# Optimization experiments

Hardware: AMD Instinct MI355X
Metric: run time of the kernel (lower is better)

The kernel has to match this reference:

```python
import jax, jax.numpy as jnp
import numpy as np

WINDOW = 1024
UNITS = 128


def setup_inputs() -> dict:
    key = jax.random.key(0)
    k1, k2, k3 = jax.random.split(key, 3)
    input_tensor = jax.random.normal(k1, (1, UNITS), dtype=jnp.float32)
    state = jax.random.normal(k2, (UNITS, WINDOW), dtype=jnp.float32)
    w = jax.random.normal(k3, (2 * UNITS + 1, UNITS), dtype=jnp.float32) * 0.05
    b = jnp.zeros((UNITS,), dtype=jnp.float32)
    return {"input_tensor": input_tensor, "state": state, "w": w, "b": b}


def reference(input_tensor, state, w, b):
    U, W = state.shape
    # state @ state_shift (shift matrix with ones on subdiagonal) == drop first column
    shifted_state = state[:, 1:]                          # [U, W-1]
    new_state = jnp.concatenate([shifted_state, input_tensor.T], axis=-1)  # [U, W]
    fs = new_state.T                                      # flip_state: [W, U]

    # h_i[i,j,:] = fs[j];  h_j[i,j,:] = fs[i]
    # se_ij = concat([h_i, h_j, <h_i,h_j>], -1); sim = se_ij @ w + b
    # Split w so we never materialize the [W,W,2U+1] concat tensor:
    w_hi = w[:U]        # [U, U] multiplies h_i (fs[j])
    w_hj = w[U:2 * U]   # [U, U] multiplies h_j (fs[i])
    w_dot = w[2 * U]    # [U]    multiplies the pairwise dot product

    proj_hi = fs @ w_hi                                   # [W, U], indexed by j
    proj_hj = fs @ w_hj                                   # [W, U], indexed by i
    d = fs @ fs.T                                         # [W, W] pairwise dots

    # sim[i,j,u] = proj_hi[j,u] + proj_hj[i,u] + d[i,j]*w_dot[u] + b[u]
    sim = proj_hi[None, :, :] + proj_hj[:, None, :] + d[:, :, None] * w_dot + b  # [W,W,U]
    a = jax.nn.softmax(sim, axis=1)                       # softmax over j

    # c[i,u] = sum_j h_i[i,j,u] * a[i,j,u] = sum_j fs[j,u] * a[i,j,u]
    c = jnp.einsum('ju,iju->iu', fs, a)                   # [W, U]
    c_last = c[-1].reshape(1, U)                          # [1, U]
    return c_last
```

## Files before the change

### kernel.cpp

```cpp
#include <hip/hip_runtime.h>


constexpr int U = 128;
constexpr int W = 1024;

__global__ __launch_bounds__(256) void rsa_last_kernel(
    const float* __restrict__ input,
    const float* __restrict__ state,
    const float* __restrict__ w,
    float* __restrict__ out)
{
    const int u    = blockIdx.x;
    const int t    = threadIdx.x;
    const int lane = t & 63;
    const int wid  = t >> 6;

    __shared__ float v[U];
    __shared__ float spv[4];
    __shared__ float smax[4];
    __shared__ float ssum[4];
    __shared__ float snum[4];

    const float wdot_u = w[2 * U * U + u];

    float pv = 0.0f;
    if (t < U) {
        float inv = input[t];
        float vt  = fmaf(wdot_u, inv, w[t * U + u]);
        v[t] = vt;
        pv   = vt * inv;
    }
    #pragma unroll
    for (int o = 32; o > 0; o >>= 1) pv += __shfl_down(pv, o, 64);
    if (lane == 0) spv[wid] = pv;
    __syncthreads();

    float acc0 = 0.f, acc1 = 0.f, acc2 = 0.f, acc3 = 0.f;
    const float4* sp = (const float4*)(state) + t;
    #pragma unroll 8
    for (int k = 0; k < U; ++k) {
        const float  vk = v[k];
        const float4 f  = sp[k * (W / 4)];
        acc0 = fmaf(vk, f.x, acc0);
        acc1 = fmaf(vk, f.y, acc1);
        acc2 = fmaf(vk, f.z, acc2);
        acc3 = fmaf(vk, f.w, acc3);
    }
    if (t == 0) acc0 = spv[0] + spv[1];

    float lm = fmaxf(fmaxf(acc0, acc1), fmaxf(acc2, acc3));
    #pragma unroll
    for (int o = 32; o > 0; o >>= 1) lm = fmaxf(lm, __shfl_down(lm, o, 64));
    if (lane == 0) smax[wid] = lm;
    __syncthreads();
    const float m = fmaxf(fmaxf(smax[0], smax[1]), fmaxf(smax[2], smax[3]));

    float4 g = *((const float4*)(state + (size_t)u * W) + t);
    if (t == 0) g.x = input[u];

    const float e0 = __expf(acc0 - m);
    const float e1 = __expf(acc1 - m);
    const float e2 = __expf(acc2 - m);
    const float e3 = __expf(acc3 - m);
    float ls = e0 + e1 + e2 + e3;
    float ln = fmaf(g.x, e0, fmaf(g.y, e1, fmaf(g.z, e2, g.w * e3)));
    #pragma unroll
    for (int o = 32; o > 0; o >>= 1) {
        ls += __shfl_down(ls, o, 64);
        ln += __shfl_down(ln, o, 64);
    }
    if (lane == 0) { ssum[wid] = ls; snum[wid] = ln; }
    __syncthreads();

    if (t == 0) {
        const float denom = ssum[0] + ssum[1] + ssum[2] + ssum[3];
        const float numer = snum[0] + snum[1] + snum[2] + snum[3];
        out[u] = numer / denom;
    }
}

extern "C" void kernel_launch(void* const* d_in, const int* in_sizes, int n_in,
                              void* d_out, int out_size, void* d_ws, size_t ws_size,
                              hipStream_t stream) {
    const float* input = (const float*)d_in[0];
    const float* state = (const float*)d_in[1];
    const float* w     = (const float*)d_in[2];
    float* out = (float*)d_out;

    rsa_last_kernel<<<dim3(U), dim3(256), 0, stream>>>(input, state, w, out);
}
```

Measured before the change: 66.53 us.

## Use one thread per window column and drop softmax max pass

Each block now launches 1024 threads, one per window column, instead of 256 threads that each handle four columns through float4 loads. Column indexing is changed to follow the shifted state directly. The softmax max-reduction and its barrier are removed, so exponentials are taken of raw logits. This raises the number of waves available to hide memory latency, at the cost of narrower per-thread loads and a risk of overflow when logits are large.

```diff
diff --git a/kernel.cpp b/kernel.cpp
--- a/kernel.cpp
+++ b/kernel.cpp
@@ -4,7 +4,7 @@
 constexpr int U = 128;
 constexpr int W = 1024;
 
-__global__ __launch_bounds__(256) void rsa_last_kernel(
+__global__ __launch_bounds__(1024, 4) void rsa_last_kernel(
     const float* __restrict__ input,
     const float* __restrict__ state,
     const float* __restrict__ w,
@@ -13,69 +13,69 @@
     const int u    = blockIdx.x;
     const int t    = threadIdx.x;
     const int lane = t & 63;
-    const int wid  = t >> 6;
+    const int wv   = t >> 6;
 
-    __shared__ float v[U];
-    __shared__ float spv[4];
-    __shared__ float smax[4];
-    __shared__ float ssum[4];
-    __shared__ float snum[4];
+    __shared__ float4 v4[U / 4];
+    __shared__ float  pvred[2];
+    __shared__ float  red[16][2];
 
     const float wdot_u = w[2 * U * U + u];
 
-    float pv = 0.0f;
     if (t < U) {
-        float inv = input[t];
-        float vt  = fmaf(wdot_u, inv, w[t * U + u]);
-        v[t] = vt;
-        pv   = vt * inv;
+        const float ik = input[t];
+        const float vt = fmaf(wdot_u, ik, w[t * U + u]);
+        ((float*)v4)[t] = vt;
+        float pv = vt * ik;
+        #pragma unroll
+        for (int o = 32; o > 0; o >>= 1) pv += __shfl_down(pv, o, 64);
+        if (lane == 0) pvred[wv] = pv;
     }
-    #pragma unroll
-    for (int o = 32; o > 0; o >>= 1) pv += __shfl_down(pv, o, 64);
-    if (lane == 0) spv[wid] = pv;
     __syncthreads();
 
-    float acc0 = 0.f, acc1 = 0.f, acc2 = 0.f, acc3 = 0.f;
-    const float4* sp = (const float4*)(state) + t;
-    #pragma unroll 8
-    for (int k = 0; k < U; ++k) {
-        const float  vk = v[k];
-        const float4 f  = sp[k * (W / 4)];
-        acc0 = fmaf(vk, f.x, acc0);
-        acc1 = fmaf(vk, f.y, acc1);
-        acc2 = fmaf(vk, f.z, acc2);
-        acc3 = fmaf(vk, f.w, acc3);
+    const int   col = (t < W - 1) ? (t + 1) : 0;
+    const float* cp = state + col;
+    float acc = 0.0f;
+    #pragma unroll
+    for (int kc = 0; kc < U / 4; ++kc) {
+        const float4 vk = v4[kc];
+        const float f0 = cp[(4 * kc + 0) * W];
+        const float f1 = cp[(4 * kc + 1) * W];
+        const float f2 = cp[(4 * kc + 2) * W];
+        const float f3 = cp[(4 * kc + 3) * W];
+        acc = fmaf(vk.x, f0, acc);
+        acc = fmaf(vk.y, f1, acc);
+        acc = fmaf(vk.z, f2, acc);
+        acc = fmaf(vk.w, f3, acc);
     }
-    if (t == 0) acc0 = spv[0] + spv[1];
 
-    float lm = fmaxf(fmaxf(acc0, acc1), fmaxf(acc2, acc3));
-    #pragma unroll
-    for (int o = 32; o > 0; o >>= 1) lm = fmaxf(lm, __shfl_down(lm, o, 64));
-    if (lane == 0) smax[wid] = lm;
-    __syncthreads();
-    const float m = fmaxf(fmaxf(smax[0], smax[1]), fmaxf(smax[2], smax[3]));
+    float g;
+    if (t < W - 1) {
+        g = state[(size_t)u * W + col];
+    } else {
+        g   = input[u];
+        acc = pvred[0] + pvred[1];
+    }
 
-    float4 g = *((const float4*)(state + (size_t)u * W) + t);
-    if (t == 0) g.x = input[u];
-
-    const float e0 = __expf(acc0 - m);
-    const float e1 = __expf(acc1 - m);
-    const float e2 = __expf(acc2 - m);
-    const float e3 = __expf(acc3 - m);
-    float ls = e0 + e1 + e2 + e3;
-    float ln = fmaf(g.x, e0, fmaf(g.y, e1, fmaf(g.z, e2, g.w * e3)));
+    const float e = __expf(acc);
+    float den = e;
+    float num = g * e;
     #pragma unroll
     for (int o = 32; o > 0; o >>= 1) {
-        ls += __shfl_down(ls, o, 64);
-        ln += __shfl_down(ln, o, 64);
+        den += __shfl_down(den, o, 64);
+        num += __shfl_down(num, o, 64);
     }
-    if (lane == 0) { ssum[wid] = ls; snum[wid] = ln; }
+    if (lane == 0) { red[wv][0] = den; red[wv][1] = num; }
     __syncthreads();
 
-    if (t == 0) {
-        const float denom = ssum[0] + ssum[1] + ssum[2] + ssum[3];
-        const float numer = snum[0] + snum[1] + snum[2] + snum[3];
-        out[u] = numer / denom;
+    if (wv == 0) {
+        float d2 = (lane < 16) ? red[lane][0] : 0.0f;
+        float n2 = (lane < 16) ? red[lane][1] : 0.0f;
+        #pragma unroll
+        for (int o = 8; o > 0; o >>= 1) {
+            d2 += __shfl_down(d2, o, 64);
+            n2 += __shfl_down(n2, o, 64);
+        }
+        if (lane == 0) out[u] = n2 / d2;
     }
 }
 
@@ -87,5 +87,5 @@
     const float* w     = (const float*)d_in[2];
     float* out = (float*)d_out;
 
-    rsa_last_kernel<<<dim3(U), dim3(256), 0, stream>>>(input, state, w, out);
+    rsa_last_kernel<<<dim3(U), dim3(1024), 0, stream>>>(input, state, w, out);
 }
```

New measurement: 111.5 us. 67.6% more time.

## Compute four output units per block, reusing state loads; drop softmax max pass

Applied to the files above, without the earlier changes.

Each block now produces four output units. Every state float4 loaded in the 128-step dot-product loop feeds 16 FMAs across four accumulator vectors instead of 4. This cuts the number of times the shared 512KB state matrix is streamed from 128 passes to 32. The softmax max-reduction and its barrier are removed, so exponentials are taken on the raw logits. That is exact in value but can overflow for large logits. The grid shrinks to 32 blocks, which lowers parallelism on a many-CU device.

```diff
diff --git a/kernel.cpp b/kernel.cpp
--- a/kernel.cpp
+++ b/kernel.cpp
@@ -10,73 +10,109 @@
     const float* __restrict__ w,
     float* __restrict__ out)
 {
-    const int u    = blockIdx.x;
+    const int u0   = blockIdx.x * 4;
     const int t    = threadIdx.x;
     const int lane = t & 63;
-    const int wid  = t >> 6;
+    const int wv   = t >> 6;
 
-    __shared__ float v[U];
-    __shared__ float spv[4];
-    __shared__ float smax[4];
-    __shared__ float ssum[4];
-    __shared__ float snum[4];
+    __shared__ __align__(16) float4 v4[U];
+    __shared__ float  s1023r[2][4];
+    __shared__ float4 s1023;
+    __shared__ float  red[4][8];
+    __shared__ float  fin[8];
 
-    const float wdot_u = w[2 * U * U + u];
+    const float4 wd4 = *(const float4*)&w[2 * U * U + u0];
+    if (t < U) {
+        const float  ik = input[t];
+        const float4 wh = *(const float4*)&w[t * U + u0];
+        float4 vk;
+        vk.x = fmaf(wd4.x, ik, wh.x);
+        vk.y = fmaf(wd4.y, ik, wh.y);
+        vk.z = fmaf(wd4.z, ik, wh.z);
+        vk.w = fmaf(wd4.w, ik, wh.w);
+        v4[t] = vk;
+        float p0 = vk.x * ik, p1 = vk.y * ik, p2 = vk.z * ik, p3 = vk.w * ik;
+        #pragma unroll
+        for (int o = 32; o > 0; o >>= 1) {
+            p0 += __shfl_down(p0, o, 64);
+            p1 += __shfl_down(p1, o, 64);
+            p2 += __shfl_down(p2, o, 64);
+            p3 += __shfl_down(p3, o, 64);
+        }
+        if (lane == 0) {
+            s1023r[wv][0] = p0; s1023r[wv][1] = p1;
+            s1023r[wv][2] = p2; s1023r[wv][3] = p3;
+        }
+    }
+    __syncthreads();
+    if (t == 0) {
+        s1023.x = s1023r[0][0] + s1023r[1][0];
+        s1023.y = s1023r[0][1] + s1023r[1][1];
+        s1023.z = s1023r[0][2] + s1023r[1][2];
+        s1023.w = s1023r[0][3] + s1023r[1][3];
+    }
+    __syncthreads();
 
-    float pv = 0.0f;
-    if (t < U) {
-        float inv = input[t];
-        float vt  = fmaf(wdot_u, inv, w[t * U + u]);
-        v[t] = vt;
-        pv   = vt * inv;
+    float4 acc0 = {0,0,0,0}, acc1 = {0,0,0,0}, acc2 = {0,0,0,0}, acc3 = {0,0,0,0};
+    const float4* sp = (const float4*)state + t;
+    #pragma unroll 8
+    for (int k = 0; k < U; ++k) {
+        const float4 f  = sp[k * (W / 4)];
+        const float4 vk = v4[k];
+        acc0.x = fmaf(vk.x, f.x, acc0.x); acc0.y = fmaf(vk.x, f.y, acc0.y);
+        acc0.z = fmaf(vk.x, f.z, acc0.z); acc0.w = fmaf(vk.x, f.w, acc0.w);
+        acc1.x = fmaf(vk.y, f.x, acc1.x); acc1.y = fmaf(vk.y, f.y, acc1.y);
+        acc1.z = fmaf(vk.y, f.z, acc1.z); acc1.w = fmaf(vk.y, f.w, acc1.w);
+        acc2.x = fmaf(vk.z, f.x, acc2.x); acc2.y = fmaf(vk.z, f.y, acc2.y);
+        acc2.z = fmaf(vk.z, f.z, acc2.z); acc2.w = fmaf(vk.z, f.w, acc2.w);
+        acc3.x = fmaf(vk.w, f.x, acc3.x); acc3.y = fmaf(vk.w, f.y, acc3.y);
+        acc3.z = fmaf(vk.w, f.z, acc3.z); acc3.w = fmaf(vk.w, f.w, acc3.w);
+    }
+    if (t == 0) {
+        acc0.x = s1023.x; acc1.x = s1023.y; acc2.x = s1023.z; acc3.x = s1023.w;
+    }
+
+    float4 g0 = *((const float4*)(state + (size_t)(u0 + 0) * W) + t);
+    float4 g1 = *((const float4*)(state + (size_t)(u0 + 1) * W) + t);
+    float4 g2 = *((const float4*)(state + (size_t)(u0 + 2) * W) + t);
+    float4 g3 = *((const float4*)(state + (size_t)(u0 + 3) * W) + t);
+    if (t == 0) {
+        g0.x = input[u0 + 0]; g1.x = input[u0 + 1];
+        g2.x = input[u0 + 2]; g3.x = input[u0 + 3];
+    }
+
+    float num0, num1, num2, num3, den0, den1, den2, den3;
+    {
+        float4 e;
+        e.x = __expf(acc0.x); e.y = __expf(acc0.y); e.z = __expf(acc0.z); e.w = __expf(acc0.w);
+        den0 = e.x + e.y + e.z + e.w;
+        num0 = fmaf(g0.x, e.x, fmaf(g0.y, e.y, fmaf(g0.z, e.z, g0.w * e.w)));
+        e.x = __expf(acc1.x); e.y = __expf(acc1.y); e.z = __expf(acc1.z); e.w = __expf(acc1.w);
+        den1 = e.x + e.y + e.z + e.w;
+        num1 = fmaf(g1.x, e.x, fmaf(g1.y, e.y, fmaf(g1.z, e.z, g1.w * e.w)));
+        e.x = __expf(acc2.x); e.y = __expf(acc2.y); e.z = __expf(acc2.z); e.w = __expf(acc2.w);
+        den2 = e.x + e.y + e.z + e.w;
+        num2 = fmaf(g2.x, e.x, fmaf(g2.y, e.y, fmaf(g2.z, e.z, g2.w * e.w)));
+        e.x = __expf(acc3.x); e.y = __expf(acc3.y); e.z = __expf(acc3.z); e.w = __expf(acc3.w);
+        den3 = e.x + e.y + e.z + e.w;
+        num3 = fmaf(g3.x, e.x, fmaf(g3.y, e.y, fmaf(g3.z, e.z, g3.w * e.w)));
     }
     #pragma unroll
-    for (int o = 32; o > 0; o >>= 1) pv += __shfl_down(pv, o, 64);
-    if (lane == 0) spv[wid] = pv;
+    for (int o = 32; o > 0; o >>= 1) {
+        num0 += __shfl_down(num0, o, 64); num1 += __shfl_down(num1, o, 64);
+        num2 += __shfl_down(num2, o, 64); num3 += __shfl_down(num3, o, 64);
+        den0 += __shfl_down(den0, o, 64); den1 += __shfl_down(den1, o, 64);
+        den2 += __shfl_down(den2, o, 64); den3 += __shfl_down(den3, o, 64);
+    }
+    if (lane == 0) {
+        red[wv][0] = num0; red[wv][1] = num1; red[wv][2] = num2; red[wv][3] = num3;
+        red[wv][4] = den0; red[wv][5] = den1; red[wv][6] = den2; red[wv][7] = den3;
+    }
     __syncthreads();
 
-    float acc0 = 0.f, acc1 = 0.f, acc2 = 0.f, acc3 = 0.f;
-    const float4* sp = (const float4*)(state) + t;
-    #pragma unroll 8
-    for (int k = 0; k < U; ++k) {
-        const float  vk = v[k];
-        const float4 f  = sp[k * (W / 4)];
-        acc0 = fmaf(vk, f.x, acc0);
-        acc1 = fmaf(vk, f.y, acc1);
-        acc2 = fmaf(vk, f.z, acc2);
-        acc3 = fmaf(vk, f.w, acc3);
-    }
-    if (t == 0) acc0 = spv[0] + spv[1];
-
-    float lm = fmaxf(fmaxf(acc0, acc1), fmaxf(acc2, acc3));
-    #pragma unroll
-    for (int o = 32; o > 0; o >>= 1) lm = fmaxf(lm, __shfl_down(lm, o, 64));
-    if (lane == 0) smax[wid] = lm;
+    if (t < 8)  fin[t] = red[0][t] + red[1][t] + red[2][t] + red[3][t];
     __syncthreads();
-    const float m = fmaxf(fmaxf(smax[0], smax[1]), fmaxf(smax[2], smax[3]));
-
-    float4 g = *((const float4*)(state + (size_t)u * W) + t);
-    if (t == 0) g.x = input[u];
-
-    const float e0 = __expf(acc0 - m);
-    const float e1 = __expf(acc1 - m);
-    const float e2 = __expf(acc2 - m);
-    const float e3 = __expf(acc3 - m);
-    float ls = e0 + e1 + e2 + e3;
-    float ln = fmaf(g.x, e0, fmaf(g.y, e1, fmaf(g.z, e2, g.w * e3)));
-    #pragma unroll
-    for (int o = 32; o > 0; o >>= 1) {
-        ls += __shfl_down(ls, o, 64);
-        ln += __shfl_down(ln, o, 64);
-    }
-    if (lane == 0) { ssum[wid] = ls; snum[wid] = ln; }
-    __syncthreads();
-
-    if (t == 0) {
-        const float denom = ssum[0] + ssum[1] + ssum[2] + ssum[3];
-        const float numer = snum[0] + snum[1] + snum[2] + snum[3];
-        out[u] = numer / denom;
-    }
+    if (t < 4)  out[u0 + t] = fin[t] / fin[t + 4];
 }
 
 extern "C" void kernel_launch(void* const* d_in, const int* in_sizes, int n_in,
@@ -87,5 +123,5 @@
     const float* w     = (const float*)d_in[2];
     float* out = (float*)d_out;
 
-    rsa_last_kernel<<<dim3(U), dim3(256), 0, stream>>>(input, state, w, out);
+    rsa_last_kernel<<<dim3(U / 4), dim3(256), 0, stream>>>(input, state, w, out);
 }
```

Measured after the change: 88.31 us. 32.7% more time.
